# Kernel optimization log

Hardware: AMD Instinct MI355X
Metric: run time of the kernel (lower is better)

Reference implementation:

```python
import jax, jax.numpy as jnp
import numpy as np


def setup_inputs() -> dict:
    key = jax.random.key(0)
    ks = jax.random.split(key, 8)
    N0, D0, E0 = 100000, 25000, 600000   # block0: src, dst, edges
    N1, D1, E1 = 25000, 5000, 120000     # block1: src, dst, edges
    IN, HID, OUT = 128, 128, 64
    h = jax.random.normal(ks[0], (N0, IN), dtype=jnp.float32)
    src0 = jax.random.randint(ks[1], (E0,), 0, N0)
    dst0 = jax.random.randint(ks[2], (E0,), 0, D0)
    src1 = jax.random.randint(ks[3], (E1,), 0, N1)
    dst1 = jax.random.randint(ks[4], (E1,), 0, D1)
    W1 = jax.random.normal(ks[5], (IN, HID), dtype=jnp.float32) / np.float32(np.sqrt(IN))
    b1 = jnp.zeros((HID,), dtype=jnp.float32)
    W2 = jax.random.normal(ks[6], (HID, OUT), dtype=jnp.float32) / np.float32(np.sqrt(HID))
    b2 = jnp.zeros((OUT,), dtype=jnp.float32)
    return dict(h=h, W1=W1, b1=b1, W2=W2, b2=b2,
                src0=src0, dst0=dst0, src1=src1, dst1=dst1,
                num_dst0=D0, num_dst1=D1)


def reference(h, W1, b1, W2, b2, src0, dst0, src1, dst1, num_dst0, num_dst1):
    # Layer 0: copy_u + sum aggregation (gather src feats, segment-sum to dst), then Linear+ReLU.
    y0 = jax.ops.segment_sum(h[src0], dst0, num_segments=num_dst0)   # [D0, IN]
    h1 = jax.nn.relu(y0 @ W1 + b1)                                   # [D0, HID]; dropout is identity at eval
    # Layer 1 (final): aggregation then Linear, no activation.
    y1 = jax.ops.segment_sum(h1[src1], dst1, num_segments=num_dst1)  # [D1, HID]
    return y1 @ W2 + b2                                              # [D1, OUT]
```

## Files before the change

kernel.cpp:

```cpp
#include <hip/hip_runtime.h>
#include <hip/hip_bf16.h>


#define D0_CONST 25000
#define D1_CONST 5000
#define LCAP 64
#define OVF_CAP 256
#define RGN_CAP 4096
#define NRANGE 236
#define GD1OFF 25088

typedef __attribute__((ext_vector_type(8))) short bf16x8;
typedef __attribute__((ext_vector_type(4))) float f32x4;
typedef __attribute__((ext_vector_type(4))) float f32x4v;
typedef __attribute__((ext_vector_type(4))) unsigned int u32x4;

__device__ __forceinline__ unsigned short f2bf(float f) {
    __hip_bfloat16 b = __float2bfloat16(f);
    return *(unsigned short*)&b;
}
__device__ __forceinline__ int swzi(int row, int e) {
    return row * 128 + (e ^ ((row & 7) << 3));
}
__device__ __forceinline__ void acc8(float* a, uint4 v) {
    a[0] += __uint_as_float(v.x << 16);
    a[1] += __uint_as_float(v.x & 0xffff0000u);
    a[2] += __uint_as_float(v.y << 16);
    a[3] += __uint_as_float(v.y & 0xffff0000u);
    a[4] += __uint_as_float(v.z << 16);
    a[5] += __uint_as_float(v.z & 0xffff0000u);
    a[6] += __uint_as_float(v.w << 16);
    a[7] += __uint_as_float(v.w & 0xffff0000u);
}
__device__ __forceinline__ f32x4v ntload_f4(const float* p) {
    return __builtin_nontemporal_load((const f32x4v*)p);
}
__device__ __forceinline__ void ntstore_u4(unsigned int* p, u32x4 v) {
    __builtin_nontemporal_store(v, (u32x4*)p);
}

__global__ __launch_bounds__(256) void prep_pack(
    const int* __restrict__ dst0, const int* __restrict__ dst1,
    unsigned short* __restrict__ gdp,
    const float* __restrict__ W1, const float* __restrict__ W2,
    unsigned short* __restrict__ W1T, unsigned short* __restrict__ W2T,
    int* __restrict__ rangecur,
    int n0, int n1)
{
    int i = blockIdx.x * 256 + threadIdx.x;
    if (i < n0) {
        int4 a = ((const int4*)dst0)[i * 2];
        int4 b = ((const int4*)dst0)[i * 2 + 1];
        u32x4 o;
        o.x = (unsigned)a.x | ((unsigned)a.y << 16);
        o.y = (unsigned)a.z | ((unsigned)a.w << 16);
        o.z = (unsigned)b.x | ((unsigned)b.y << 16);
        o.w = (unsigned)b.z | ((unsigned)b.w << 16);
        ((u32x4*)gdp)[i] = o;
    } else if (i < n0 + n1) {
        int j = i - n0;
        int4 a = ((const int4*)dst1)[j * 2];
        int4 b = ((const int4*)dst1)[j * 2 + 1];
        u32x4 o;
        o.x = (unsigned)(a.x + GD1OFF) | ((unsigned)(a.y + GD1OFF) << 16);
        o.y = (unsigned)(a.z + GD1OFF) | ((unsigned)(a.w + GD1OFF) << 16);
        o.z = (unsigned)(b.x + GD1OFF) | ((unsigned)(b.y + GD1OFF) << 16);
        o.w = (unsigned)(b.z + GD1OFF) | ((unsigned)(b.w + GD1OFF) << 16);
        ((u32x4*)gdp)[i] = o;
    } else {
        int j = i - n0 - n1;
        if (j < 128 * 128) {
            int k = j >> 7, n = j & 127;
            W1T[n * 128 + k] = f2bf(W1[j]);
        } else if (j < 128 * 128 + 128 * 64) {
            int j2 = j - 128 * 128;
            int k = j2 >> 6, n = j2 & 63;
            W2T[n * 128 + k] = f2bf(W2[j2]);
        } else {
            int k2 = j - 128 * 128 - 128 * 64;
            if (k2 < NRANGE) rangecur[k2] = k2 * RGN_CAP;
        }
    }
}

__global__ __launch_bounds__(256) void scatter_cast(
    const unsigned short* __restrict__ gdp,
    const int* __restrict__ src0, const int* __restrict__ src1,
    int E0, int ET,
    int* __restrict__ rgn, int* __restrict__ rangecur,
    const float* __restrict__ hf, unsigned int* __restrict__ hbf, int n8,
    int nbScat)
{
    __shared__ int hist[256];
    __shared__ int base[256];

    int b = blockIdx.x, t = threadIdx.x;
    if (b < nbScat) {
        hist[t] = 0;
        __syncthreads();

        int eb = b * 4096 + t * 16;
        const u32x4* gv = (const u32x4*)gdp;
        u32x4 p0 = gv[(size_t)b * 512 + t * 2];
        u32x4 p1 = gv[(size_t)b * 512 + t * 2 + 1];
        unsigned wa[8] = {p0.x, p0.y, p0.z, p0.w, p1.x, p1.y, p1.z, p1.w};
        int g[16], rk[16], dl[16];
        #pragma unroll
        for (int k = 0; k < 16; ++k) {
            unsigned gd = (wa[k >> 1] >> ((k & 1) * 16)) & 0xffffu;
            g[k]  = (int)(gd >> 7);
            dl[k] = (int)(gd & 127u);
            rk[k] = (eb + k < ET) ? atomicAdd(&hist[g[k]], 1) : 0;
        }
        __syncthreads();
        if (t < NRANGE) {
            int c = hist[t];
            base[t] = c ? atomicAdd(&rangecur[t], c) : 0;
        }
        __syncthreads();

        int s[16];
        if (eb + 16 <= E0) {
            #pragma unroll
            for (int q = 0; q < 4; ++q) {
                int4 v = ((const int4*)(src0 + eb))[q];
                s[q * 4] = v.x; s[q * 4 + 1] = v.y; s[q * 4 + 2] = v.z; s[q * 4 + 3] = v.w;
            }
        } else if (eb >= E0 && eb + 16 <= ET) {
            const int* sp = src1 + (eb - E0);
            #pragma unroll
            for (int q = 0; q < 4; ++q) {
                int4 v = ((const int4*)sp)[q];
                s[q * 4] = v.x; s[q * 4 + 1] = v.y; s[q * 4 + 2] = v.z; s[q * 4 + 3] = v.w;
            }
        } else {
            #pragma unroll
            for (int k = 0; k < 16; ++k) {
                int e = eb + k;
                s[k] = (e < E0) ? src0[e] : ((e < ET) ? src1[e - E0] : 0);
            }
        }

        #pragma unroll
        for (int k = 0; k < 16; ++k) {
            int e = eb + k;
            if (e < ET) {
                int pos = base[g[k]] + rk[k];
                if (pos < (g[k] + 1) * RGN_CAP)
                    rgn[pos] = (dl[k] << 17) | s[k];
            }
        }
    } else {
        int i = (b - nbScat) * 256 + t;
        if (i < n8) {
            f32x4v a = ntload_f4(hf + (size_t)i * 8);
            f32x4v c = ntload_f4(hf + (size_t)i * 8 + 4);
            u32x4 o;
            o.x = f2bf(a.x) | ((unsigned)f2bf(a.y) << 16);
            o.y = f2bf(a.z) | ((unsigned)f2bf(a.w) << 16);
            o.z = f2bf(c.x) | ((unsigned)f2bf(c.y) << 16);
            o.w = f2bf(c.z) | ((unsigned)f2bf(c.w) << 16);
            ntstore_u4(hbf + (size_t)i * 4, o);
        }
    }
}

__global__ __launch_bounds__(256) void build_csr(
    const int* __restrict__ rgn, const int* __restrict__ rangecur,
    int* __restrict__ bktc,
    int* __restrict__ cnt,
    int* __restrict__ ovf, int* __restrict__ ovfc)
{
    __shared__ int lists[128 * LCAP];
    __shared__ int lcnt[128];
    __shared__ int lovf[OVF_CAP];
    __shared__ int lovfc;

    int g = blockIdx.x, t = threadIdx.x;
    if (t < 128) lcnt[t] = 0;
    if (t == 0) lovfc = 0;
    __syncthreads();

    int n = rangecur[g] - g * RGN_CAP;
    if (n > RGN_CAP) n = RGN_CAP;
    const int* rp = rgn + (size_t)g * RGN_CAP;
    for (int i = t; i < n; i += 256) {
        int e = rp[i];
        int dl = e >> 17;
        int s  = e & 0x1FFFF;
        int r = atomicAdd(&lcnt[dl], 1);
        if (r < LCAP) lists[(dl << 6) + r] = s;
        else {
            int p2 = atomicAdd(&lovfc, 1);
            if (p2 < OVF_CAP) lovf[p2] = (dl << 24) | s;
        }
    }
    __syncthreads();

    if (t < 128) cnt[g * 128 + t] = lcnt[t];
    if (t == 0) ovfc[g] = (lovfc > OVF_CAP) ? OVF_CAP : lovfc;
    for (int i = t; i < 128 * LCAP / 4; i += 256)
        ((uint4*)bktc)[(size_t)g * (128 * LCAP / 4) + i] = ((const uint4*)lists)[i];
    int no = lovfc; if (no > OVF_CAP) no = OVF_CAP;
    for (int i = t; i < no; i += 256) ovf[g * OVF_CAP + i] = lovf[i];
}

__global__ __launch_bounds__(256) void gather0_kernel(
    const uint4* __restrict__ x,
    const int* __restrict__ bktc, const int* __restrict__ cntg,
    const int* __restrict__ ovfg, const int* __restrict__ ovfcg,
    uint4* __restrict__ y,
    int D)
{
    int tid = blockIdx.x * 256 + threadIdx.x;
    int d = tid >> 3;
    int c = tid & 7;
    if (d >= D) return;
    int n = cntg[d];
    int base = d << 6;
    int nl = (n > LCAP) ? LCAP : n;

    float a[16];
    #pragma unroll
    for (int q = 0; q < 16; ++q) a[q] = 0.f;

    int i = 0;
    for (; i + 4 <= nl; i += 4) {
        int4 s4 = *(const int4*)&bktc[base + i];
        uint4 v0a = x[(size_t)s4.x * 16 + c * 2];
        uint4 v0b = x[(size_t)s4.x * 16 + c * 2 + 1];
        uint4 v1a = x[(size_t)s4.y * 16 + c * 2];
        uint4 v1b = x[(size_t)s4.y * 16 + c * 2 + 1];
        uint4 v2a = x[(size_t)s4.z * 16 + c * 2];
        uint4 v2b = x[(size_t)s4.z * 16 + c * 2 + 1];
        uint4 v3a = x[(size_t)s4.w * 16 + c * 2];
        uint4 v3b = x[(size_t)s4.w * 16 + c * 2 + 1];
        acc8(a, v0a); acc8(a + 8, v0b);
        acc8(a, v1a); acc8(a + 8, v1b);
        acc8(a, v2a); acc8(a + 8, v2b);
        acc8(a, v3a); acc8(a + 8, v3b);
    }
    for (; i < nl; ++i) {
        int s0 = bktc[base + i];
        acc8(a,     x[(size_t)s0 * 16 + c * 2]);
        acc8(a + 8, x[(size_t)s0 * 16 + c * 2 + 1]);
    }
    if (n > LCAP) {
        int br = d >> 7;
        int no = ovfcg[br];
        int dl = d & 127;
        for (int k = 0; k < no; ++k) {
            int e = ovfg[(br << 8) + k];
            if ((e >> 24) == dl) {
                int s0 = e & 0xFFFFFF;
                acc8(a,     x[(size_t)s0 * 16 + c * 2]);
                acc8(a + 8, x[(size_t)s0 * 16 + c * 2 + 1]);
            }
        }
    }

    uint4 o0, o1;
    o0.x = f2bf(a[0])  | ((unsigned)f2bf(a[1])  << 16);
    o0.y = f2bf(a[2])  | ((unsigned)f2bf(a[3])  << 16);
    o0.z = f2bf(a[4])  | ((unsigned)f2bf(a[5])  << 16);
    o0.w = f2bf(a[6])  | ((unsigned)f2bf(a[7])  << 16);
    o1.x = f2bf(a[8])  | ((unsigned)f2bf(a[9])  << 16);
    o1.y = f2bf(a[10]) | ((unsigned)f2bf(a[11]) << 16);
    o1.z = f2bf(a[12]) | ((unsigned)f2bf(a[13]) << 16);
    o1.w = f2bf(a[14]) | ((unsigned)f2bf(a[15]) << 16);
    y[(size_t)d * 16 + c * 2]     = o0;
    y[(size_t)d * 16 + c * 2 + 1] = o1;
}

__global__ __launch_bounds__(256) void fused_linear(
    const unsigned short* __restrict__ y0bf,
    const unsigned short* __restrict__ W1T,
    const unsigned short* __restrict__ W2T,
    const float* __restrict__ b1,
    unsigned short* __restrict__ t,
    int M)
{
    __shared__ unsigned short Ys[128 * 128];
    __shared__ unsigned short W1s[128 * 128];
    __shared__ unsigned short W2s[64 * 128];

    int tid = threadIdx.x;
    int r0 = blockIdx.x * 128;

    for (int idx = tid; idx < 2048; idx += 256) {
        int r = idx >> 4, ch = idx & 15;
        uint4 v = make_uint4(0, 0, 0, 0);
        if (r0 + r < M) v = *(const uint4*)&y0bf[(size_t)(r0 + r) * 128 + ch * 8];
        *(uint4*)&Ys[swzi(r, ch * 8)] = v;
    }
    for (int idx = tid; idx < 2048; idx += 256) {
        int r = idx >> 4, ch = idx & 15;
        *(uint4*)&W1s[swzi(r, ch * 8)] = *(const uint4*)&W1T[r * 128 + ch * 8];
    }
    for (int idx = tid; idx < 1024; idx += 256) {
        int r = idx >> 4, ch = idx & 15;
        *(uint4*)&W2s[swzi(r, ch * 8)] = *(const uint4*)&W2T[r * 128 + ch * 8];
    }
    __syncthreads();

    int w = tid >> 6, lane = tid & 63;
    int lr = lane & 15, lhi = lane >> 4;
    int wr = 32 * w;

    bf16x8 a[2][4];
    #pragma unroll
    for (int m = 0; m < 2; ++m)
        #pragma unroll
        for (int kt = 0; kt < 4; ++kt)
            a[m][kt] = *(bf16x8*)&Ys[swzi(wr + 16 * m + lr, kt * 32 + lhi * 8)];

    f32x4 acc1[2][8];
    #pragma unroll
    for (int m = 0; m < 2; ++m)
        #pragma unroll
        for (int ct = 0; ct < 8; ++ct) acc1[m][ct] = (f32x4)(0.f);

    #pragma unroll
    for (int ct = 0; ct < 8; ++ct) {
        #pragma unroll
        for (int kt = 0; kt < 4; ++kt) {
            bf16x8 b = *(bf16x8*)&W1s[swzi(ct * 16 + lr, kt * 32 + lhi * 8)];
            acc1[0][ct] = __builtin_amdgcn_mfma_f32_16x16x32_bf16(a[0][kt], b, acc1[0][ct], 0, 0, 0);
            acc1[1][ct] = __builtin_amdgcn_mfma_f32_16x16x32_bf16(a[1][kt], b, acc1[1][ct], 0, 0, 0);
        }
    }

    #pragma unroll
    for (int ct = 0; ct < 8; ++ct) {
        float bv = b1[ct * 16 + lr];
        #pragma unroll
        for (int m = 0; m < 2; ++m)
            #pragma unroll
            for (int q = 0; q < 4; ++q) {
                float v = fmaxf(acc1[m][ct][q] + bv, 0.f);
                Ys[swzi(wr + 16 * m + lhi * 4 + q, ct * 16 + lr)] = f2bf(v);
            }
    }

    bf16x8 a2[2][4];
    #pragma unroll
    for (int m = 0; m < 2; ++m)
        #pragma unroll
        for (int kt = 0; kt < 4; ++kt)
            a2[m][kt] = *(bf16x8*)&Ys[swzi(wr + 16 * m + lr, kt * 32 + lhi * 8)];

    f32x4 acc2[2][4];
    #pragma unroll
    for (int m = 0; m < 2; ++m)
        #pragma unroll
        for (int ct = 0; ct < 4; ++ct) acc2[m][ct] = (f32x4)(0.f);

    #pragma unroll
    for (int ct = 0; ct < 4; ++ct) {
        #pragma unroll
        for (int kt = 0; kt < 4; ++kt) {
            bf16x8 b = *(bf16x8*)&W2s[swzi(ct * 16 + lr, kt * 32 + lhi * 8)];
            acc2[0][ct] = __builtin_amdgcn_mfma_f32_16x16x32_bf16(a2[0][kt], b, acc2[0][ct], 0, 0, 0);
            acc2[1][ct] = __builtin_amdgcn_mfma_f32_16x16x32_bf16(a2[1][kt], b, acc2[1][ct], 0, 0, 0);
        }
    }

    #pragma unroll
    for (int m = 0; m < 2; ++m)
        #pragma unroll
        for (int ct = 0; ct < 4; ++ct)
            #pragma unroll
            for (int q = 0; q < 4; ++q) {
                int row = r0 + wr + 16 * m + lhi * 4 + q;
                if (row < M) t[(size_t)row * 64 + ct * 16 + lr] = f2bf(acc2[m][ct][q]);
            }
}

__global__ __launch_bounds__(256) void gather1_kernel(
    const uint4* __restrict__ x,
    const int* __restrict__ bktc, const int* __restrict__ cntg,
    const int* __restrict__ ovfg, const int* __restrict__ ovfcg,
    const float* __restrict__ b2,
    float4* __restrict__ out,
    int D)
{
    int tid = blockIdx.x * 256 + threadIdx.x;
    int d = tid >> 3;
    int c = tid & 7;
    if (d >= D) return;
    int gd = GD1OFF + d;
    int n = cntg[gd];
    int base = gd << 6;
    int nl = (n > LCAP) ? LCAP : n;

    float a[8] = {0.f, 0.f, 0.f, 0.f, 0.f, 0.f, 0.f, 0.f};
    int i = 0;
    for (; i + 4 <= nl; i += 4) {
        int4 s4 = *(const int4*)&bktc[base + i];
        uint4 v0 = x[(size_t)s4.x * 8 + c];
        uint4 v1 = x[(size_t)s4.y * 8 + c];
        uint4 v2 = x[(size_t)s4.z * 8 + c];
        uint4 v3 = x[(size_t)s4.w * 8 + c];
        acc8(a, v0); acc8(a, v1); acc8(a, v2); acc8(a, v3);
    }
    for (; i < nl; ++i) acc8(a, x[(size_t)bktc[base + i] * 8 + c]);
    if (n > LCAP) {
        int br = gd >> 7;
        int no = ovfcg[br];
        int dl = gd & 127;
        for (int k = 0; k < no; ++k) {
            int e = ovfg[(br << 8) + k];
            if ((e >> 24) == dl) acc8(a, x[(size_t)(e & 0xFFFFFF) * 8 + c]);
        }
    }

    float4 blo = *(const float4*)&b2[c * 8];
    float4 bhi = *(const float4*)&b2[c * 8 + 4];
    float4 o0 = make_float4(a[0] + blo.x, a[1] + blo.y, a[2] + blo.z, a[3] + blo.w);
    float4 o1 = make_float4(a[4] + bhi.x, a[5] + bhi.y, a[6] + bhi.z, a[7] + bhi.w);
    out[(size_t)d * 16 + c * 2]     = o0;
    out[(size_t)d * 16 + c * 2 + 1] = o1;
}

extern "C" void kernel_launch(void* const* d_in, const int* in_sizes, int n_in,
                              void* d_out, int out_size, void* d_ws, size_t ws_size,
                              hipStream_t stream) {
    const float* h    = (const float*)d_in[0];
    const float* W1   = (const float*)d_in[1];
    const float* b1   = (const float*)d_in[2];
    const float* W2   = (const float*)d_in[3];
    const float* b2   = (const float*)d_in[4];
    const int*   src0 = (const int*)d_in[5];
    const int*   dst0 = (const int*)d_in[6];
    const int*   src1 = (const int*)d_in[7];
    const int*   dst1 = (const int*)d_in[8];

    const int N0 = in_sizes[0] / 128;
    const int E0 = in_sizes[5];
    const int E1 = in_sizes[7];
    const int ET = E0 + E1;
    const int D0 = D0_CONST;
    const int D1 = D1_CONST;
    const int nbScat = (ET + 4095) / 4096;

    char* p = (char*)d_ws;
    unsigned short* hbf  = (unsigned short*)p; p += (size_t)N0 * 128 * 2;
    unsigned short* y0bf = (unsigned short*)p; p += (size_t)D0 * 128 * 2;
    unsigned short* tbf  = (unsigned short*)p; p += (size_t)D0 * 64 * 2;
    unsigned short* W1T  = (unsigned short*)p; p += 128 * 128 * 2;
    unsigned short* W2T  = (unsigned short*)p; p += 64 * 128 * 2;
    unsigned short* gdp  = (unsigned short*)p; p += (size_t)nbScat * 4096 * 2;
    int* rgn      = (int*)p; p += (size_t)NRANGE * RGN_CAP * 4;
    int* bktc     = (int*)p; p += (size_t)NRANGE * 128 * LCAP * 4;
    int* cntg     = (int*)p; p += (size_t)NRANGE * 128 * 4;
    int* rangecur = (int*)p; p += 256 * 4;
    int* ovf      = (int*)p; p += (size_t)NRANGE * OVF_CAP * 4;
    int* ovfc     = (int*)p; p += 256 * 4;

    float* out = (float*)d_out;

    {
        int n0 = E0 / 8, n1 = E1 / 8;
        int tot = n0 + n1 + 128 * 128 + 128 * 64 + NRANGE;
        prep_pack<<<(tot + 255) / 256, 256, 0, stream>>>(
            dst0, dst1, gdp, W1, W2, W1T, W2T, rangecur, n0, n1);
    }

    {
        int n8 = N0 * 128 / 8;
        int castBlocks = (n8 + 255) / 256;
        scatter_cast<<<nbScat + castBlocks, 256, 0, stream>>>(
            gdp, src0, src1, E0, ET, rgn, rangecur,
            h, (unsigned int*)hbf, n8, nbScat);
    }

    build_csr<<<NRANGE, 256, 0, stream>>>(rgn, rangecur, bktc, cntg, ovf, ovfc);

    {
        long long threads = (long long)D0 * 8;
        gather0_kernel<<<(int)((threads + 255) / 256), 256, 0, stream>>>(
            (const uint4*)hbf, bktc, cntg, ovf, ovfc, (uint4*)y0bf, D0);
    }
    fused_linear<<<(D0 + 127) / 128, 256, 0, stream>>>(y0bf, W1T, W2T, b1, tbf, D0);

    {
        long long threads = (long long)D1 * 8;
        gather1_kernel<<<(int)((threads + 255) / 256), 256, 0, stream>>>(
            (const uint4*)tbf, bktc, cntg, ovf, ovfc, b2, (float4*)out, D1);
    }
}
```

Baseline: 84.53 us.

## Fuse CSR build, layer-0 gather and MLP into one per-32-row kernel

Removes the separate build_csr kernel and the y0bf intermediate. Each 32-row block now filters its 128-row range bucket from rgn into shared-memory lists, gathers and sums the bf16 source features, and runs both MFMA linears directly on the result. gather1 likewise builds its own lists from rgn. This saves two launches and the global round trips for bktc, cnt and y0. The cost is that every range bucket is scanned four times, W1T and W2T are read from global memory instead of LDS, and the overflow capacity per block is smaller.

New measurement: 75.13 us, median of 2. 11.1% less time.

```diff
diff --git a/kernel.cpp b/kernel.cpp
--- a/kernel.cpp
+++ b/kernel.cpp
@@ -5,7 +5,7 @@
 #define D0_CONST 25000
 #define D1_CONST 5000
 #define LCAP 64
-#define OVF_CAP 256
+#define OVFB 64
 #define RGN_CAP 4096
 #define NRANGE 236
 #define GD1OFF 25088
@@ -91,12 +91,12 @@
     const float* __restrict__ hf, unsigned int* __restrict__ hbf, int n8,
     int nbScat)
 {
-    __shared__ int hist[256];
-    __shared__ int base[256];
+    __shared__ int hist[512];
+    __shared__ int base[512];
 
     int b = blockIdx.x, t = threadIdx.x;
     if (b < nbScat) {
-        hist[t] = 0;
+        hist[t] = 0; hist[t + 256] = 0;
         __syncthreads();
 
         int eb = b * 4096 + t * 16;
@@ -165,253 +165,227 @@
     }
 }
 
-__global__ __launch_bounds__(256) void build_csr(
+__global__ __launch_bounds__(256) void gather0_linear(
+    const uint4* __restrict__ x,
     const int* __restrict__ rgn, const int* __restrict__ rangecur,
-    int* __restrict__ bktc,
-    int* __restrict__ cnt,
-    int* __restrict__ ovf, int* __restrict__ ovfc)
-{
-    __shared__ int lists[128 * LCAP];
-    __shared__ int lcnt[128];
-    __shared__ int lovf[OVF_CAP];
-    __shared__ int lovfc;
-
-    int g = blockIdx.x, t = threadIdx.x;
-    if (t < 128) lcnt[t] = 0;
-    if (t == 0) lovfc = 0;
-    __syncthreads();
-
-    int n = rangecur[g] - g * RGN_CAP;
-    if (n > RGN_CAP) n = RGN_CAP;
-    const int* rp = rgn + (size_t)g * RGN_CAP;
-    for (int i = t; i < n; i += 256) {
-        int e = rp[i];
-        int dl = e >> 17;
-        int s  = e & 0x1FFFF;
-        int r = atomicAdd(&lcnt[dl], 1);
-        if (r < LCAP) lists[(dl << 6) + r] = s;
-        else {
-            int p2 = atomicAdd(&lovfc, 1);
-            if (p2 < OVF_CAP) lovf[p2] = (dl << 24) | s;
-        }
-    }
-    __syncthreads();
-
-    if (t < 128) cnt[g * 128 + t] = lcnt[t];
-    if (t == 0) ovfc[g] = (lovfc > OVF_CAP) ? OVF_CAP : lovfc;
-    for (int i = t; i < 128 * LCAP / 4; i += 256)
-        ((uint4*)bktc)[(size_t)g * (128 * LCAP / 4) + i] = ((const uint4*)lists)[i];
-    int no = lovfc; if (no > OVF_CAP) no = OVF_CAP;
-    for (int i = t; i < no; i += 256) ovf[g * OVF_CAP + i] = lovf[i];
-}
-
-__global__ __launch_bounds__(256) void gather0_kernel(
-    const uint4* __restrict__ x,
-    const int* __restrict__ bktc, const int* __restrict__ cntg,
-    const int* __restrict__ ovfg, const int* __restrict__ ovfcg,
-    uint4* __restrict__ y,
-    int D)
-{
-    int tid = blockIdx.x * 256 + threadIdx.x;
-    int d = tid >> 3;
-    int c = tid & 7;
-    if (d >= D) return;
-    int n = cntg[d];
-    int base = d << 6;
-    int nl = (n > LCAP) ? LCAP : n;
-
-    float a[16];
-    #pragma unroll
-    for (int q = 0; q < 16; ++q) a[q] = 0.f;
-
-    int i = 0;
-    for (; i + 4 <= nl; i += 4) {
-        int4 s4 = *(const int4*)&bktc[base + i];
-        uint4 v0a = x[(size_t)s4.x * 16 + c * 2];
-        uint4 v0b = x[(size_t)s4.x * 16 + c * 2 + 1];
-        uint4 v1a = x[(size_t)s4.y * 16 + c * 2];
-        uint4 v1b = x[(size_t)s4.y * 16 + c * 2 + 1];
-        uint4 v2a = x[(size_t)s4.z * 16 + c * 2];
-        uint4 v2b = x[(size_t)s4.z * 16 + c * 2 + 1];
-        uint4 v3a = x[(size_t)s4.w * 16 + c * 2];
-        uint4 v3b = x[(size_t)s4.w * 16 + c * 2 + 1];
-        acc8(a, v0a); acc8(a + 8, v0b);
-        acc8(a, v1a); acc8(a + 8, v1b);
-        acc8(a, v2a); acc8(a + 8, v2b);
-        acc8(a, v3a); acc8(a + 8, v3b);
-    }
-    for (; i < nl; ++i) {
-        int s0 = bktc[base + i];
-        acc8(a,     x[(size_t)s0 * 16 + c * 2]);
-        acc8(a + 8, x[(size_t)s0 * 16 + c * 2 + 1]);
-    }
-    if (n > LCAP) {
-        int br = d >> 7;
-        int no = ovfcg[br];
-        int dl = d & 127;
-        for (int k = 0; k < no; ++k) {
-            int e = ovfg[(br << 8) + k];
-            if ((e >> 24) == dl) {
-                int s0 = e & 0xFFFFFF;
-                acc8(a,     x[(size_t)s0 * 16 + c * 2]);
-                acc8(a + 8, x[(size_t)s0 * 16 + c * 2 + 1]);
-            }
-        }
-    }
-
-    uint4 o0, o1;
-    o0.x = f2bf(a[0])  | ((unsigned)f2bf(a[1])  << 16);
-    o0.y = f2bf(a[2])  | ((unsigned)f2bf(a[3])  << 16);
-    o0.z = f2bf(a[4])  | ((unsigned)f2bf(a[5])  << 16);
-    o0.w = f2bf(a[6])  | ((unsigned)f2bf(a[7])  << 16);
-    o1.x = f2bf(a[8])  | ((unsigned)f2bf(a[9])  << 16);
-    o1.y = f2bf(a[10]) | ((unsigned)f2bf(a[11]) << 16);
-    o1.z = f2bf(a[12]) | ((unsigned)f2bf(a[13]) << 16);
-    o1.w = f2bf(a[14]) | ((unsigned)f2bf(a[15]) << 16);
-    y[(size_t)d * 16 + c * 2]     = o0;
-    y[(size_t)d * 16 + c * 2 + 1] = o1;
-}
-
-__global__ __launch_bounds__(256) void fused_linear(
-    const unsigned short* __restrict__ y0bf,
     const unsigned short* __restrict__ W1T,
     const unsigned short* __restrict__ W2T,
     const float* __restrict__ b1,
     unsigned short* __restrict__ t,
     int M)
 {
-    __shared__ unsigned short Ys[128 * 128];
-    __shared__ unsigned short W1s[128 * 128];
-    __shared__ unsigned short W2s[64 * 128];
-
-    int tid = threadIdx.x;
-    int r0 = blockIdx.x * 128;
-
-    for (int idx = tid; idx < 2048; idx += 256) {
-        int r = idx >> 4, ch = idx & 15;
-        uint4 v = make_uint4(0, 0, 0, 0);
-        if (r0 + r < M) v = *(const uint4*)&y0bf[(size_t)(r0 + r) * 128 + ch * 8];
-        *(uint4*)&Ys[swzi(r, ch * 8)] = v;
-    }
-    for (int idx = tid; idx < 2048; idx += 256) {
-        int r = idx >> 4, ch = idx & 15;
-        *(uint4*)&W1s[swzi(r, ch * 8)] = *(const uint4*)&W1T[r * 128 + ch * 8];
-    }
-    for (int idx = tid; idx < 1024; idx += 256) {
-        int r = idx >> 4, ch = idx & 15;
-        *(uint4*)&W2s[swzi(r, ch * 8)] = *(const uint4*)&W2T[r * 128 + ch * 8];
+    __shared__ int lists[32 * LCAP];
+    __shared__ int lcnt[32];
+    __shared__ int lovf[OVFB];
+    __shared__ int lovfc;
+    __shared__ unsigned short Ys[32 * 128];
+    __shared__ unsigned short H1s[32 * 128];
+
+    int b = blockIdx.x, tid = threadIdx.x;
+    int row0 = b * 32;
+    int g = row0 >> 7;
+    int sub = (row0 >> 5) & 3;
+
+    if (tid < 32) lcnt[tid] = 0;
+    if (tid == 0) lovfc = 0;
+    __syncthreads();
+
+    int n = rangecur[g] - g * RGN_CAP;
+    if (n > RGN_CAP) n = RGN_CAP;
+    const int* rp = rgn + (size_t)g * RGN_CAP;
+    for (int i = tid; i < n; i += 256) {
+        int e = rp[i];
+        if ((e >> 22) == sub) {
+            int dl = (e >> 17) & 31;
+            int s  = e & 0x1FFFF;
+            int r = atomicAdd(&lcnt[dl], 1);
+            if (r < LCAP) lists[(dl << 6) + r] = s;
+            else {
+                int p2 = atomicAdd(&lovfc, 1);
+                if (p2 < OVFB) lovf[p2] = (dl << 17) | s;
+            }
+        }
+    }
+    __syncthreads();
+
+    {
+        int lrow = tid >> 3, c = tid & 7;
+        int nn = lcnt[lrow]; if (nn > LCAP) nn = LCAP;
+        const int* lp = &lists[lrow << 6];
+        float a[16];
+        #pragma unroll
+        for (int q = 0; q < 16; ++q) a[q] = 0.f;
+
+        int i = 0;
+        for (; i + 4 <= nn; i += 4) {
+            int4 s4 = *(const int4*)&lp[i];
+            uint4 v0a = x[(size_t)s4.x * 16 + c * 2];
+            uint4 v0b = x[(size_t)s4.x * 16 + c * 2 + 1];
+            uint4 v1a = x[(size_t)s4.y * 16 + c * 2];
+            uint4 v1b = x[(size_t)s4.y * 16 + c * 2 + 1];
+            uint4 v2a = x[(size_t)s4.z * 16 + c * 2];
+            uint4 v2b = x[(size_t)s4.z * 16 + c * 2 + 1];
+            uint4 v3a = x[(size_t)s4.w * 16 + c * 2];
+            uint4 v3b = x[(size_t)s4.w * 16 + c * 2 + 1];
+            acc8(a, v0a); acc8(a + 8, v0b);
+            acc8(a, v1a); acc8(a + 8, v1b);
+            acc8(a, v2a); acc8(a + 8, v2b);
+            acc8(a, v3a); acc8(a + 8, v3b);
+        }
+        for (; i < nn; ++i) {
+            int s0 = lp[i];
+            acc8(a,     x[(size_t)s0 * 16 + c * 2]);
+            acc8(a + 8, x[(size_t)s0 * 16 + c * 2 + 1]);
+        }
+        int no = lovfc; if (no > OVFB) no = OVFB;
+        for (int k2 = 0; k2 < no; ++k2) {
+            int e = lovf[k2];
+            if ((e >> 17) == lrow) {
+                int s0 = e & 0x1FFFF;
+                acc8(a,     x[(size_t)s0 * 16 + c * 2]);
+                acc8(a + 8, x[(size_t)s0 * 16 + c * 2 + 1]);
+            }
+        }
+        uint4 o0, o1;
+        o0.x = f2bf(a[0])  | ((unsigned)f2bf(a[1])  << 16);
+        o0.y = f2bf(a[2])  | ((unsigned)f2bf(a[3])  << 16);
+        o0.z = f2bf(a[4])  | ((unsigned)f2bf(a[5])  << 16);
+        o0.w = f2bf(a[6])  | ((unsigned)f2bf(a[7])  << 16);
+        o1.x = f2bf(a[8])  | ((unsigned)f2bf(a[9])  << 16);
+        o1.y = f2bf(a[10]) | ((unsigned)f2bf(a[11]) << 16);
+        o1.z = f2bf(a[12]) | ((unsigned)f2bf(a[13]) << 16);
+        o1.w = f2bf(a[14]) | ((unsigned)f2bf(a[15]) << 16);
+        *(uint4*)&Ys[swzi(lrow, c * 16)]     = o0;
+        *(uint4*)&Ys[swzi(lrow, c * 16 + 8)] = o1;
     }
     __syncthreads();
 
     int w = tid >> 6, lane = tid & 63;
     int lr = lane & 15, lhi = lane >> 4;
-    int wr = 32 * w;
-
-    bf16x8 a[2][4];
+
+    bf16x8 a1[2][4];
     #pragma unroll
     for (int m = 0; m < 2; ++m)
         #pragma unroll
         for (int kt = 0; kt < 4; ++kt)
-            a[m][kt] = *(bf16x8*)&Ys[swzi(wr + 16 * m + lr, kt * 32 + lhi * 8)];
-
-    f32x4 acc1[2][8];
+            a1[m][kt] = *(bf16x8*)&Ys[swzi(16 * m + lr, kt * 32 + lhi * 8)];
+
+    f32x4 acc1[2][2];
     #pragma unroll
     for (int m = 0; m < 2; ++m)
         #pragma unroll
-        for (int ct = 0; ct < 8; ++ct) acc1[m][ct] = (f32x4)(0.f);
-
-    #pragma unroll
-    for (int ct = 0; ct < 8; ++ct) {
+        for (int j = 0; j < 2; ++j) acc1[m][j] = (f32x4)(0.f);
+
+    #pragma unroll
+    for (int j = 0; j < 2; ++j) {
+        int ct = 2 * w + j;
         #pragma unroll
         for (int kt = 0; kt < 4; ++kt) {
-            bf16x8 b = *(bf16x8*)&W1s[swzi(ct * 16 + lr, kt * 32 + lhi * 8)];
-            acc1[0][ct] = __builtin_amdgcn_mfma_f32_16x16x32_bf16(a[0][kt], b, acc1[0][ct], 0, 0, 0);
-            acc1[1][ct] = __builtin_amdgcn_mfma_f32_16x16x32_bf16(a[1][kt], b, acc1[1][ct], 0, 0, 0);
-        }
-    }
-
-    #pragma unroll
-    for (int ct = 0; ct < 8; ++ct) {
+            bf16x8 bb = *(const bf16x8*)&W1T[(ct * 16 + lr) * 128 + kt * 32 + lhi * 8];
+            acc1[0][j] = __builtin_amdgcn_mfma_f32_16x16x32_bf16(a1[0][kt], bb, acc1[0][j], 0, 0, 0);
+            acc1[1][j] = __builtin_amdgcn_mfma_f32_16x16x32_bf16(a1[1][kt], bb, acc1[1][j], 0, 0, 0);
+        }
+    }
+
+    #pragma unroll
+    for (int j = 0; j < 2; ++j) {
+        int ct = 2 * w + j;
         float bv = b1[ct * 16 + lr];
         #pragma unroll
         for (int m = 0; m < 2; ++m)
             #pragma unroll
             for (int q = 0; q < 4; ++q) {
-                float v = fmaxf(acc1[m][ct][q] + bv, 0.f);
-                Ys[swzi(wr + 16 * m + lhi * 4 + q, ct * 16 + lr)] = f2bf(v);
-            }
-    }
+                float v = fmaxf(acc1[m][j][q] + bv, 0.f);
+                H1s[swzi(16 * m + lhi * 4 + q, ct * 16 + lr)] = f2bf(v);
+            }
+    }
+    __syncthreads();
 
     bf16x8 a2[2][4];
     #pragma unroll
     for (int m = 0; m < 2; ++m)
         #pragma unroll
         for (int kt = 0; kt < 4; ++kt)
-            a2[m][kt] = *(bf16x8*)&Ys[swzi(wr + 16 * m + lr, kt * 32 + lhi * 8)];
-
-    f32x4 acc2[2][4];
+            a2[m][kt] = *(bf16x8*)&H1s[swzi(16 * m + lr, kt * 32 + lhi * 8)];
+
+    f32x4 acc2[2];
+    acc2[0] = (f32x4)(0.f); acc2[1] = (f32x4)(0.f);
+    #pragma unroll
+    for (int kt = 0; kt < 4; ++kt) {
+        bf16x8 bb = *(const bf16x8*)&W2T[(w * 16 + lr) * 128 + kt * 32 + lhi * 8];
+        acc2[0] = __builtin_amdgcn_mfma_f32_16x16x32_bf16(a2[0][kt], bb, acc2[0], 0, 0, 0);
+        acc2[1] = __builtin_amdgcn_mfma_f32_16x16x32_bf16(a2[1][kt], bb, acc2[1], 0, 0, 0);
+    }
+
     #pragma unroll
     for (int m = 0; m < 2; ++m)
         #pragma unroll
-        for (int ct = 0; ct < 4; ++ct) acc2[m][ct] = (f32x4)(0.f);
-
-    #pragma unroll
-    for (int ct = 0; ct < 4; ++ct) {
-        #pragma unroll
-        for (int kt = 0; kt < 4; ++kt) {
-            bf16x8 b = *(bf16x8*)&W2s[swzi(ct * 16 + lr, kt * 32 + lhi * 8)];
-            acc2[0][ct] = __builtin_amdgcn_mfma_f32_16x16x32_bf16(a2[0][kt], b, acc2[0][ct], 0, 0, 0);
-            acc2[1][ct] = __builtin_amdgcn_mfma_f32_16x16x32_bf16(a2[1][kt], b, acc2[1][ct], 0, 0, 0);
-        }
-    }
-
-    #pragma unroll
-    for (int m = 0; m < 2; ++m)
-        #pragma unroll
-        for (int ct = 0; ct < 4; ++ct)
-            #pragma unroll
-            for (int q = 0; q < 4; ++q) {
-                int row = r0 + wr + 16 * m + lhi * 4 + q;
-                if (row < M) t[(size_t)row * 64 + ct * 16 + lr] = f2bf(acc2[m][ct][q]);
-            }
+        for (int q = 0; q < 4; ++q) {
+            int row = row0 + 16 * m + lhi * 4 + q;
+            if (row < M) t[(size_t)row * 64 + w * 16 + lr] = f2bf(acc2[m][q]);
+        }
 }
 
 __global__ __launch_bounds__(256) void gather1_kernel(
     const uint4* __restrict__ x,
-    const int* __restrict__ bktc, const int* __restrict__ cntg,
-    const int* __restrict__ ovfg, const int* __restrict__ ovfcg,
+    const int* __restrict__ rgn, const int* __restrict__ rangecur,
     const float* __restrict__ b2,
     float4* __restrict__ out,
     int D)
 {
-    int tid = blockIdx.x * 256 + threadIdx.x;
-    int d = tid >> 3;
-    int c = tid & 7;
+    __shared__ int lists[32 * LCAP];
+    __shared__ int lcnt[32];
+    __shared__ int lovf[OVFB];
+    __shared__ int lovfc;
+
+    int b = blockIdx.x, tid = threadIdx.x;
+    int row0 = b * 32;
+    int g = 196 + (row0 >> 7);
+    int sub = (row0 >> 5) & 3;
+
+    if (tid < 32) lcnt[tid] = 0;
+    if (tid == 0) lovfc = 0;
+    __syncthreads();
+
+    int n = rangecur[g] - g * RGN_CAP;
+    if (n > RGN_CAP) n = RGN_CAP;
+    const int* rp = rgn + (size_t)g * RGN_CAP;
+    for (int i = tid; i < n; i += 256) {
+        int e = rp[i];
+        if ((e >> 22) == sub) {
+            int dl = (e >> 17) & 31;
+            int s  = e & 0x1FFFF;
+            int r = atomicAdd(&lcnt[dl], 1);
+            if (r < LCAP) lists[(dl << 6) + r] = s;
+            else {
+                int p2 = atomicAdd(&lovfc, 1);
+                if (p2 < OVFB) lovf[p2] = (dl << 17) | s;
+            }
+        }
+    }
+    __syncthreads();
+
+    int lrow = tid >> 3, c = tid & 7;
+    int d = row0 + lrow;
     if (d >= D) return;
-    int gd = GD1OFF + d;
-    int n = cntg[gd];
-    int base = gd << 6;
-    int nl = (n > LCAP) ? LCAP : n;
+    int nn = lcnt[lrow]; if (nn > LCAP) nn = LCAP;
+    const int* lp = &lists[lrow << 6];
 
     float a[8] = {0.f, 0.f, 0.f, 0.f, 0.f, 0.f, 0.f, 0.f};
     int i = 0;
-    for (; i + 4 <= nl; i += 4) {
-        int4 s4 = *(const int4*)&bktc[base + i];
+    for (; i + 4 <= nn; i += 4) {
+        int4 s4 = *(const int4*)&lp[i];
         uint4 v0 = x[(size_t)s4.x * 8 + c];
         uint4 v1 = x[(size_t)s4.y * 8 + c];
         uint4 v2 = x[(size_t)s4.z * 8 + c];
         uint4 v3 = x[(size_t)s4.w * 8 + c];
         acc8(a, v0); acc8(a, v1); acc8(a, v2); acc8(a, v3);
     }
-    for (; i < nl; ++i) acc8(a, x[(size_t)bktc[base + i] * 8 + c]);
-    if (n > LCAP) {
-        int br = gd >> 7;
-        int no = ovfcg[br];
-        int dl = gd & 127;
-        for (int k = 0; k < no; ++k) {
-            int e = ovfg[(br << 8) + k];
-            if ((e >> 24) == dl) acc8(a, x[(size_t)(e & 0xFFFFFF) * 8 + c]);
-        }
+    for (; i < nn; ++i) acc8(a, x[(size_t)lp[i] * 8 + c]);
+    int no = lovfc; if (no > OVFB) no = OVFB;
+    for (int k2 = 0; k2 < no; ++k2) {
+        int e = lovf[k2];
+        if ((e >> 17) == lrow) acc8(a, x[(size_t)(e & 0x1FFFF) * 8 + c]);
     }
 
     float4 blo = *(const float4*)&b2[c * 8];
@@ -445,17 +419,12 @@
 
     char* p = (char*)d_ws;
     unsigned short* hbf  = (unsigned short*)p; p += (size_t)N0 * 128 * 2;
-    unsigned short* y0bf = (unsigned short*)p; p += (size_t)D0 * 128 * 2;
     unsigned short* tbf  = (unsigned short*)p; p += (size_t)D0 * 64 * 2;
     unsigned short* W1T  = (unsigned short*)p; p += 128 * 128 * 2;
     unsigned short* W2T  = (unsigned short*)p; p += 64 * 128 * 2;
     unsigned short* gdp  = (unsigned short*)p; p += (size_t)nbScat * 4096 * 2;
     int* rgn      = (int*)p; p += (size_t)NRANGE * RGN_CAP * 4;
-    int* bktc     = (int*)p; p += (size_t)NRANGE * 128 * LCAP * 4;
-    int* cntg     = (int*)p; p += (size_t)NRANGE * 128 * 4;
     int* rangecur = (int*)p; p += 256 * 4;
-    int* ovf      = (int*)p; p += (size_t)NRANGE * OVF_CAP * 4;
-    int* ovfc     = (int*)p; p += 256 * 4;
 
     float* out = (float*)d_out;
 
@@ -474,18 +443,15 @@
             h, (unsigned int*)hbf, n8, nbScat);
     }
 
-    build_csr<<<NRANGE, 256, 0, stream>>>(rgn, rangecur, bktc, cntg, ovf, ovfc);
-
     {
-        long long threads = (long long)D0 * 8;
-        gather0_kernel<<<(int)((threads + 255) / 256), 256, 0, stream>>>(
-            (const uint4*)hbf, bktc, cntg, ovf, ovfc, (uint4*)y0bf, D0);
-    }
-    fused_linear<<<(D0 + 127) / 128, 256, 0, stream>>>(y0bf, W1T, W2T, b1, tbf, D0);
+        int blocks = (D0 + 31) / 32;
+        gather0_linear<<<blocks, 256, 0, stream>>>(
+            (const uint4*)hbf, rgn, rangecur, W1T, W2T, b1, tbf, D0);
+    }
 
     {
-        long long threads = (long long)D1 * 8;
-        gather1_kernel<<<(int)((threads + 255) / 256), 256, 0, stream>>>(
-            (const uint4*)tbf, bktc, cntg, ovf, ovfc, b2, (float4*)out, D1);
-    }
-}
+        int blocks = (D1 + 31) / 32;
+        gather1_kernel<<<blocks, 256, 0, stream>>>(
+            (const uint4*)tbf, rgn, rangecur, b2, (float4*)out, D1);
+    }
+}
```
